# Optimization experiments

Measured on AMD Instinct MI355X. Metric: run time of the kernel, lower is better.

Reference implementation:

```python
import jax, jax.numpy as jnp
import numpy as np

GROUP_SIZE = 128


def dequant_rtn(qweight, scale, zero_point):
    # qweight: [O, I] int, scale/zero_point: [O, I//GROUP_SIZE]
    O, I = qweight.shape
    G = scale.shape[1]
    gs = I // G
    q = qweight.reshape(O, G, gs).astype(jnp.float32)
    zp = zero_point.astype(jnp.float32)[:, :, None]
    w = (q - zp) * scale[:, :, None]
    return w.reshape(O, I)


def setup_inputs() -> dict:
    key = jax.random.key(0)
    k1, k2, k3, k4, k5 = jax.random.split(key, 5)
    B, S, I, O = 2, 2048, 4096, 11008
    G = I // GROUP_SIZE
    x = jax.random.normal(k1, (B, S, I), dtype=jnp.float32)
    qweight = jax.random.randint(k2, (O, I), 0, 16, dtype=jnp.int32)
    scale = jax.random.uniform(k3, (O, G), dtype=jnp.float32) * 0.02 + 1e-3
    zero_point = jax.random.randint(k4, (O, G), 0, 16, dtype=jnp.int32)
    bias = jax.random.normal(k5, (O,), dtype=jnp.float32)
    return {"x": x, "qweight": qweight, "scale": scale,
            "zero_point": zero_point, "bias": bias}


def reference(x, qweight, scale, zero_point, bias):
    # weight-only path: dequant weight, then F.linear(x, w, bias)
    w = dequant_rtn(qweight, scale, zero_point)  # [O, I] fp32
    return jnp.einsum('bsi,oi->bso', x, w) + bias
```

## Files before the change

kernel.cpp:

```cpp
#include <hip/hip_runtime.h>
#include <cstdint>
#include <cstddef>

typedef __attribute__((ext_vector_type(4))) int i32x4;
typedef __bf16 bf16;
typedef __attribute__((ext_vector_type(8))) __bf16 bf16x8;
typedef __attribute__((ext_vector_type(4))) float f32x4;

#define BM 128
#define BN 128
#define BKB 128
#define GROUP_M 16
#define GM256 4
#define NXCD 8

__device__ __forceinline__ unsigned bf16_rne(float f) {
  unsigned u = __float_as_uint(f);
  unsigned r = 0x7FFFu + ((u >> 16) & 1u);
  return ((u + r) >> 16) & 0xFFFFu;
}
__device__ __forceinline__ unsigned pack2(float a, float b) {
  return bf16_rne(a) | (bf16_rne(b) << 16);
}
__device__ __forceinline__ int pack4i8(int a, int b, int c, int d) {
  return (a & 0xFF) | ((b & 0xFF) << 8) | ((c & 0xFF) << 16) | (d << 24);
}
__device__ __forceinline__ int q_i8(float v) {
  v = fminf(fmaxf(v, -127.0f), 127.0f);
  return __float2int_rn(v);
}

__global__ __launch_bounds__(256) void prep_kernel(
    const float* __restrict__ x, char* __restrict__ xq, float* __restrict__ xscale,
    int M,
    const int* __restrict__ q, const float* __restrict__ scale,
    const int* __restrict__ zp, char* __restrict__ wq, float* __restrict__ wscale,
    int K, int G) {
  __shared__ float red[4];
  const int b = blockIdx.x;
  const int tid = threadIdx.x;
  float f[16];

  if (b < M) {
    const float4* src = (const float4*)(x + (size_t)b * K);
#pragma unroll
    for (int i = 0; i < 4; ++i) {
      float4 v = src[tid + 256 * i];
      f[4 * i + 0] = v.x; f[4 * i + 1] = v.y;
      f[4 * i + 2] = v.z; f[4 * i + 3] = v.w;
    }
  } else {
    const int row = b - M;
    const int4* src = (const int4*)(q + (size_t)row * K);
    const float* srow = scale + (size_t)row * G;
    const int*   zrow = zp + (size_t)row * G;
#pragma unroll
    for (int i = 0; i < 4; ++i) {
      const int j = tid + 256 * i;
      const int g = j >> 5;
      const float s = srow[g];
      const float nzs = -s * (float)zrow[g];
      int4 qv = src[j];
      f[4 * i + 0] = fmaf((float)qv.x, s, nzs);
      f[4 * i + 1] = fmaf((float)qv.y, s, nzs);
      f[4 * i + 2] = fmaf((float)qv.z, s, nzs);
      f[4 * i + 3] = fmaf((float)qv.w, s, nzs);
    }
  }

  float m = 0.f;
#pragma unroll
  for (int j = 0; j < 16; ++j) m = fmaxf(m, fabsf(f[j]));
#pragma unroll
  for (int off = 32; off >= 1; off >>= 1) m = fmaxf(m, __shfl_xor(m, off));
  if ((tid & 63) == 0) red[tid >> 6] = m;
  __syncthreads();
  m = fmaxf(fmaxf(red[0], red[1]), fmaxf(red[2], red[3]));

  const float inv = m > 0.f ? 127.0f / m : 0.f;
  int pk[4];
#pragma unroll
  for (int i = 0; i < 4; ++i)
    pk[i] = pack4i8(q_i8(f[4 * i + 0] * inv), q_i8(f[4 * i + 1] * inv),
                    q_i8(f[4 * i + 2] * inv), q_i8(f[4 * i + 3] * inv));

  char* dst = (b < M) ? (xq + (size_t)b * K) : (wq + (size_t)(b - M) * K);
  int* dst_i32 = (int*)dst;
#pragma unroll
  for (int i = 0; i < 4; ++i) dst_i32[tid + 256 * i] = pk[i];

  if (tid == 0) {
    if (b < M) xscale[b] = m * (1.0f / 127.0f);
    else       wscale[b - M] = m * (1.0f / 127.0f);
  }
}

typedef __attribute__((address_space(1))) void gas_void;
typedef __attribute__((address_space(3))) void las_void;

__device__ __forceinline__ void load_lds16(const void* g, void* l) {
  __builtin_amdgcn_global_load_lds((gas_void*)g, (las_void*)l, 16, 0, 0);
}


#define STAGE_A(buf, half, ktb) do {                                          \
    load_lds16(A + abase + (size_t)(half) * 128 * K + (size_t)(ktb) + off0,   \
               &Al[buf][(half) * 16384 + d0w]);                               \
    load_lds16(A + abase + (size_t)(half) * 128 * K + (size_t)(ktb) + off1,   \
               &Al[buf][(half) * 16384 + d1w]);                               \
  } while (0)

#define STAGE_B(buf, half, ktb) do {                                          \
    load_lds16(Bw + bbase + (size_t)(half) * 128 * K + (size_t)(ktb) + off0,  \
               &Bl[buf][(half) * 16384 + d0w]);                               \
    load_lds16(Bw + bbase + (size_t)(half) * 128 * K + (size_t)(ktb) + off1,  \
               &Bl[buf][(half) * 16384 + d1w]);                               \
  } while (0)

#define PHASE(CUR, MH, NH, STAGE_STMT, WAIT_STMT) do {                        \
    i32x4 afr[4][2], bfr[2][2];                                               \
    _Pragma("unroll")                                                         \
    for (int tm = 0; tm < 4; ++tm) {                                          \
      _Pragma("unroll")                                                       \
      for (int ks = 0; ks < 2; ++ks) {                                        \
        int row = wmb + (MH) * 64 + tm * 16 + l16;                            \
        int kq  = ks * 4 + quad;                                              \
        afr[tm][ks] =                                                         \
            *(const i32x4*)&Al[CUR][(row * 8 + (kq ^ (row & 7))) * 16];       \
      }                                                                       \
    }                                                                         \
    _Pragma("unroll")                                                         \
    for (int tn = 0; tn < 2; ++tn) {                                          \
      _Pragma("unroll")                                                       \
      for (int ks = 0; ks < 2; ++ks) {                                        \
        int row = wnb + (NH) * 32 + tn * 16 + l16;                            \
        int kq  = ks * 4 + quad;                                              \
        bfr[tn][ks] =                                                         \
            *(const i32x4*)&Bl[CUR][(row * 8 + (kq ^ (row & 7))) * 16];       \
      }                                                                       \
    }                                                                         \
    STAGE_STMT;                                                               \
    __builtin_amdgcn_s_barrier();                                             \
    asm volatile("s_waitcnt lgkmcnt(0)" ::: "memory");                        \
    __builtin_amdgcn_sched_barrier(0);                                        \
    __builtin_amdgcn_s_setprio(1);                                            \
    _Pragma("unroll")                                                         \
    for (int tm = 0; tm < 4; ++tm) {                                          \
      _Pragma("unroll")                                                       \
      for (int tn = 0; tn < 2; ++tn) {                                        \
        _Pragma("unroll")                                                     \
        for (int ks = 0; ks < 2; ++ks) {                                      \
          acc[(MH) * 4 + tm][(NH) * 2 + tn] =                                 \
              __builtin_amdgcn_mfma_i32_16x16x64_i8(                          \
                  afr[tm][ks], bfr[tn][ks],                                   \
                  acc[(MH) * 4 + tm][(NH) * 2 + tn], 0, 0, 0);                \
        }                                                                     \
      }                                                                       \
    }                                                                         \
    __builtin_amdgcn_s_setprio(0);                                            \
    WAIT_STMT;                                                                \
    __builtin_amdgcn_s_barrier();                                             \
    __builtin_amdgcn_sched_barrier(0);                                        \
  } while (0)

__global__ __launch_bounds__(512) void gemm_i8_256(
    const char* __restrict__ A,
    const char* __restrict__ Bw,
    const float* __restrict__ ascale,
    const float* __restrict__ bscale,
    const float* __restrict__ bias,
    float* __restrict__ C,
    int M, int N, int K) {
  __shared__ __align__(16) char Al[2][256 * 128];
  __shared__ __align__(16) char Bl[2][256 * 128];
  const int tid  = threadIdx.x;
  const int wave = tid >> 6;
  const int lane = tid & 63;
  const int quad = lane >> 4;
  const int l16  = lane & 15;
  const int wmb  = (wave >> 2) * 128;
  const int wnb  = (wave & 3) * 64;

  const int nbm = M / 256, nbn = N / 256;
  const int cpx = (nbm * nbn) / NXCD;
  const int swz = ((int)blockIdx.x % NXCD) * cpx + (int)blockIdx.x / NXCD;
  const int per_group = GM256 * nbn;
  const int gid = swz / per_group;
  const int rem = swz - gid * per_group;
  int gm = nbm - gid * GM256; if (gm > GM256) gm = GM256;
  const int bm = (gid * GM256 + (rem % gm)) * 256;
  const int bn = (rem / gm) * 256;

  const int sA = tid, sB = 512 + tid;
  const int m0 = sA >> 3, m1 = sB >> 3;
  const size_t off0 = (size_t)m0 * K + (size_t)(((sA & 7) ^ (m0 & 7)) * 16);
  const size_t off1 = (size_t)m1 * K + (size_t)(((sB & 7) ^ (m1 & 7)) * 16);
  const int d0w = (0 * 512 + wave * 64) * 16;
  const int d1w = (1 * 512 + wave * 64) * 16;
  const size_t abase = (size_t)bm * K;
  const size_t bbase = (size_t)bn * K;
  const int NT = K / 128;

  i32x4 acc[8][4];
#pragma unroll
  for (int i = 0; i < 8; ++i)
#pragma unroll
    for (int j = 0; j < 4; ++j)
      acc[i][j] = (i32x4){0, 0, 0, 0};

  STAGE_A(0, 0, 0);
  STAGE_A(0, 1, 0);
  STAGE_B(0, 0, 0);
  STAGE_B(0, 1, 0);
  asm volatile("s_waitcnt vmcnt(0)" ::: "memory");
  __builtin_amdgcn_s_barrier();
  __builtin_amdgcn_sched_barrier(0);

  for (int t = 0; t < NT; ++t) {
    const int cur = t & 1;
    const int nxt = cur ^ 1;
    const int kt1 = (t + 1) * 128;
    const bool s1 = (t + 1) < NT;

    PHASE(cur, 0, 0, { if (s1) { STAGE_A(nxt, 0, kt1); STAGE_A(nxt, 1, kt1); } }, {});
    PHASE(cur, 1, 0, { if (s1) { STAGE_B(nxt, 0, kt1); STAGE_B(nxt, 1, kt1); } }, {});
    PHASE(cur, 0, 1, {}, {});
    PHASE(cur, 1, 1, {},
          { asm volatile("s_waitcnt vmcnt(0)" ::: "memory"); });
  }

#pragma unroll
  for (int tn = 0; tn < 4; ++tn) {
    int col = bn + wnb + tn * 16 + l16;
    float bv = bias[col];
    float ws = bscale[col];
#pragma unroll
    for (int tm = 0; tm < 8; ++tm) {
      int row0 = bm + wmb + tm * 16 + quad * 4;
#pragma unroll
      for (int v = 0; v < 4; ++v) {
        float val = ascale[row0 + v] * ws * (float)acc[tm][tn][v] + bv;
        __builtin_nontemporal_store(val, &C[(size_t)(row0 + v) * N + col]);
      }
    }
  }
}

__global__ __launch_bounds__(256) void gemm_i8_kernel(
    const char* __restrict__ A, const char* __restrict__ Bw,
    const float* __restrict__ ascale, const float* __restrict__ bscale,
    const float* __restrict__ bias, float* __restrict__ C,
    int M, int N, int K) {
  __shared__ __align__(16) char Alds[BM * BKB];
  __shared__ __align__(16) char Blds[BN * BKB];
  const int tid  = threadIdx.x;
  const int wave = tid >> 6;
  const int lane = tid & 63;
  const int quad = lane >> 4;
  const int l16  = lane & 15;

  const int nbm = M / BM;
  const int nbn = N / BN;
  int flat = blockIdx.x;
  int per_group = GROUP_M * nbn;
  int gid = flat / per_group;
  int rem = flat - gid * per_group;
  int gm = nbm - gid * GROUP_M;
  if (gm > GROUP_M) gm = GROUP_M;
  const int bm = (gid * GROUP_M + (rem % gm)) * BM;
  const int bn = (rem / gm) * BN;

  const int wm = (wave & 1) * 64;
  const int wn = (wave >> 1) * 64;

  i32x4 acc[4][4];
#pragma unroll
  for (int i = 0; i < 4; ++i)
#pragma unroll
    for (int j = 0; j < 4; ++j)
      acc[i][j] = (i32x4){0, 0, 0, 0};

  for (int kt = 0; kt < K; kt += BKB) {
#pragma unroll
    for (int t = 0; t < 4; ++t) {
      int s0 = (wave * 4 + t) * 64;
      int s  = s0 + lane;
      int m  = s >> 3;
      int kq = (s & 7) ^ (m & 7);
      load_lds16(A  + (size_t)(bm + m) * K + kt + kq * 16, &Alds[s0 * 16]);
      load_lds16(Bw + (size_t)(bn + m) * K + kt + kq * 16, &Blds[s0 * 16]);
    }
    __syncthreads();

#pragma unroll
    for (int ks = 0; ks < 2; ++ks) {
      i32x4 af[4], bfr[4];
#pragma unroll
      for (int tm = 0; tm < 4; ++tm) {
        int m  = wm + tm * 16 + l16;
        int kq = ks * 4 + quad;
        af[tm] = *(const i32x4*)&Alds[(m * 8 + (kq ^ (m & 7))) * 16];
      }
#pragma unroll
      for (int tn = 0; tn < 4; ++tn) {
        int n  = wn + tn * 16 + l16;
        int kq = ks * 4 + quad;
        bfr[tn] = *(const i32x4*)&Blds[(n * 8 + (kq ^ (n & 7))) * 16];
      }
#pragma unroll
      for (int tm = 0; tm < 4; ++tm)
#pragma unroll
        for (int tn = 0; tn < 4; ++tn)
          acc[tm][tn] = __builtin_amdgcn_mfma_i32_16x16x64_i8(
              af[tm], bfr[tn], acc[tm][tn], 0, 0, 0);
    }
    __syncthreads();
  }

#pragma unroll
  for (int tn = 0; tn < 4; ++tn) {
    int col = bn + wn + tn * 16 + l16;
    float bv = bias[col];
    float ws = bscale[col];
#pragma unroll
    for (int tm = 0; tm < 4; ++tm) {
      int row0 = bm + wm + tm * 16 + quad * 4;
#pragma unroll
      for (int v = 0; v < 4; ++v) {
        float val = ascale[row0 + v] * ws * (float)acc[tm][tn][v] + bv;
        __builtin_nontemporal_store(val, &C[(size_t)(row0 + v) * N + col]);
      }
    }
  }
}

__global__ __launch_bounds__(256) void gemm_fused_kernel(
    const float* __restrict__ X, const int* __restrict__ Q,
    const float* __restrict__ scale, const int* __restrict__ zp,
    const float* __restrict__ bias, float* __restrict__ C,
    int M, int N, int K, int G) {
  __shared__ __align__(16) bf16 Alds[128 * 64];
  __shared__ __align__(16) bf16 Blds[128 * 64];
  const int tid  = threadIdx.x;
  const int wave = tid >> 6;
  const int lane = tid & 63;
  const int quad = lane >> 4;
  const int l16  = lane & 15;
  const int bm = blockIdx.y * 128;
  const int bn = blockIdx.x * 128;
  const int wm = (wave & 1) * 64;
  const int wn = (wave >> 1) * 64;

  f32x4 acc[4][4];
#pragma unroll
  for (int i = 0; i < 4; ++i)
#pragma unroll
    for (int j = 0; j < 4; ++j)
      acc[i][j] = (f32x4){0.f, 0.f, 0.f, 0.f};

  for (int kt = 0; kt < K; kt += 64) {
#pragma unroll
    for (int i = 0; i < 4; ++i) {
      int c = tid + i * 256;
      int m = c >> 3;
      int kq = (c & 7) ^ (m & 7);
      const float* src = X + (size_t)(bm + m) * K + kt + kq * 8;
      float4 v0 = *(const float4*)src;
      float4 v1 = *(const float4*)(src + 4);
      uint4 p;
      p.x = pack2(v0.x, v0.y); p.y = pack2(v0.z, v0.w);
      p.z = pack2(v1.x, v1.y); p.w = pack2(v1.z, v1.w);
      *(uint4*)&Alds[c * 8] = p;
    }
#pragma unroll
    for (int i = 0; i < 4; ++i) {
      int c = tid + i * 256;
      int n = c >> 3;
      int kq = (c & 7) ^ (n & 7);
      int kcol = kt + kq * 8;
      size_t row = (size_t)(bn + n);
      int g = kcol >> 7;
      float s = scale[row * G + g];
      float z = (float)zp[row * G + g];
      const int* src = Q + row * K + kcol;
      int4 q0 = *(const int4*)src;
      int4 q1 = *(const int4*)(src + 4);
      uint4 p;
      p.x = pack2(((float)q0.x - z) * s, ((float)q0.y - z) * s);
      p.y = pack2(((float)q0.z - z) * s, ((float)q0.w - z) * s);
      p.z = pack2(((float)q1.x - z) * s, ((float)q1.y - z) * s);
      p.w = pack2(((float)q1.z - z) * s, ((float)q1.w - z) * s);
      *(uint4*)&Blds[c * 8] = p;
    }
    __syncthreads();

#pragma unroll
    for (int ks = 0; ks < 2; ++ks) {
      bf16x8 af[4], bfr[4];
#pragma unroll
      for (int tm = 0; tm < 4; ++tm) {
        int m  = wm + tm * 16 + l16;
        int kq = ks * 4 + quad;
        af[tm] = *(const bf16x8*)&Alds[(m * 8 + (kq ^ (m & 7))) * 8];
      }
#pragma unroll
      for (int tn = 0; tn < 4; ++tn) {
        int n  = wn + tn * 16 + l16;
        int kq = ks * 4 + quad;
        bfr[tn] = *(const bf16x8*)&Blds[(n * 8 + (kq ^ (n & 7))) * 8];
      }
#pragma unroll
      for (int tm = 0; tm < 4; ++tm)
#pragma unroll
        for (int tn = 0; tn < 4; ++tn)
          acc[tm][tn] = __builtin_amdgcn_mfma_f32_16x16x32_bf16(
              af[tm], bfr[tn], acc[tm][tn], 0, 0, 0);
    }
    __syncthreads();
  }

#pragma unroll
  for (int tn = 0; tn < 4; ++tn) {
    int col = bn + wn + tn * 16 + l16;
    float bv = bias[col];
#pragma unroll
    for (int tm = 0; tm < 4; ++tm) {
      int row0 = bm + wm + tm * 16 + quad * 4;
#pragma unroll
      for (int v = 0; v < 4; ++v)
        C[(size_t)(row0 + v) * N + col] = acc[tm][tn][v] + bv;
    }
  }
}

extern "C" void kernel_launch(void* const* d_in, const int* in_sizes, int n_in,
                              void* d_out, int out_size, void* d_ws, size_t ws_size,
                              hipStream_t stream) {
  const float* x     = (const float*)d_in[0];
  const int*   qw    = (const int*)d_in[1];
  const float* scale = (const float*)d_in[2];
  const int*   zp    = (const int*)d_in[3];
  const float* bias  = (const float*)d_in[4];
  float* out = (float*)d_out;

  const int O = in_sizes[4];
  const int I = (int)(in_sizes[1] / O);
  const int M = (int)(in_sizes[0] / I);
  const int G = in_sizes[2] / O;
  const int K = I, N = O;

  size_t off_xq = 0;
  size_t off_xs = off_xq + (size_t)M * K;
  size_t off_wq = (off_xs + (size_t)M * 4 + 255) & ~(size_t)255;
  size_t off_ws_ = off_wq + (size_t)N * K;
  size_t need   = ((off_ws_ + (size_t)N * 4 + 255) & ~(size_t)255);

  if (ws_size >= need && K == 4096) {
    char*  xq = (char*)d_ws + off_xq;
    float* xs = (float*)((char*)d_ws + off_xs);
    char*  wq = (char*)d_ws + off_wq;
    float* wsc = (float*)((char*)d_ws + off_ws_);

    prep_kernel<<<M + N, 256, 0, stream>>>(x, xq, xs, M, qw, scale, zp, wq, wsc, K, G);

    const int nb256 = (M / 256) * (N / 256);
    if ((M % 256) == 0 && (N % 256) == 0 && (nb256 % NXCD) == 0) {
      gemm_i8_256<<<nb256, 512, 0, stream>>>(xq, wq, xs, wsc, bias, out, M, N, K);
    } else {
      int nblocks = (M / BM) * (N / BN);
      gemm_i8_kernel<<<nblocks, 256, 0, stream>>>(xq, wq, xs, wsc, bias, out, M, N, K);
    }
  } else {
    dim3 gemm_grid((unsigned)(N / 128), (unsigned)(M / 128));
    gemm_fused_kernel<<<gemm_grid, 256, 0, stream>>>(x, qw, scale, zp, bias, out,
                                                     M, N, K, G);
  }
}
```

Baseline: 557.5 us.

## Split LDS tiles into quarter-stages and prefetch two K-steps ahead

Reorganizes the A and B LDS layouts into halves indexed by which phase consumes them. Each half is refilled as soon as the phase reading it finishes, so the loads for step t+2 are issued into the current buffer while step t is still computing. The waits become partial (vmcnt(4)) instead of full drains, which deepens the pipeline and hides more global load latency. The cost is more involved buffer-reuse ordering, which relies on correct barrier placement to avoid overwriting data before every wave has read it.

Result: no change. 563.2 us (+1.0%).

```diff
diff --git a/kernel.cpp b/kernel.cpp
--- a/kernel.cpp
+++ b/kernel.cpp
@@ -103,18 +103,18 @@
 }
 
 
-#define STAGE_A(buf, half, ktb) do {                                          \
-    load_lds16(A + abase + (size_t)(half) * 128 * K + (size_t)(ktb) + off0,   \
-               &Al[buf][(half) * 16384 + d0w]);                               \
-    load_lds16(A + abase + (size_t)(half) * 128 * K + (size_t)(ktb) + off1,   \
-               &Al[buf][(half) * 16384 + d1w]);                               \
+#define STAGE_A_H(buf, h, ktb) do {                                           \
+    load_lds16(A + abase + (size_t)(ktb) + aoff0 + (size_t)(h) * 64 * K,      \
+               &Al[buf][(h) * 8192 + dw]);                                    \
+    load_lds16(A + abase + (size_t)(ktb) + aoff1 + (size_t)(h) * 64 * K,      \
+               &Al[buf][16384 + (h) * 8192 + dw]);                            \
   } while (0)
 
-#define STAGE_B(buf, half, ktb) do {                                          \
-    load_lds16(Bw + bbase + (size_t)(half) * 128 * K + (size_t)(ktb) + off0,  \
-               &Bl[buf][(half) * 16384 + d0w]);                               \
-    load_lds16(Bw + bbase + (size_t)(half) * 128 * K + (size_t)(ktb) + off1,  \
-               &Bl[buf][(half) * 16384 + d1w]);                               \
+#define STAGE_B_H(buf, h, ktb) do {                                           \
+    load_lds16(Bw + bbase + (size_t)(ktb) + boff0 + (size_t)(h) * 32 * K,     \
+               &Bl[buf][(h) * 16384 + dw]);                                   \
+    load_lds16(Bw + bbase + (size_t)(ktb) + boff1 + (size_t)(h) * 32 * K,     \
+               &Bl[buf][(h) * 16384 + 8192 + dw]);                            \
   } while (0)
 
 #define PHASE(CUR, MH, NH, STAGE_STMT, WAIT_STMT) do {                        \
@@ -133,10 +133,10 @@
     for (int tn = 0; tn < 2; ++tn) {                                          \
       _Pragma("unroll")                                                       \
       for (int ks = 0; ks < 2; ++ks) {                                        \
-        int row = wnb + (NH) * 32 + tn * 16 + l16;                            \
-        int kq  = ks * 4 + quad;                                              \
+        int p  = (NH) * 128 + wq3 * 32 + tn * 16 + l16;                       \
+        int kq = ks * 4 + quad;                                               \
         bfr[tn][ks] =                                                         \
-            *(const i32x4*)&Bl[CUR][(row * 8 + (kq ^ (row & 7))) * 16];       \
+            *(const i32x4*)&Bl[CUR][(p * 8 + (kq ^ (p & 7))) * 16];           \
       }                                                                       \
     }                                                                         \
     STAGE_STMT;                                                               \
@@ -178,8 +178,9 @@
   const int lane = tid & 63;
   const int quad = lane >> 4;
   const int l16  = lane & 15;
+  const int wq3  = wave & 3;
   const int wmb  = (wave >> 2) * 128;
-  const int wnb  = (wave & 3) * 64;
+  const int wnb  = wq3 * 64;
 
   const int nbm = M / 256, nbn = N / 256;
   const int cpx = (nbm * nbn) / NXCD;
@@ -191,12 +192,13 @@
   const int bm = (gid * GM256 + (rem % gm)) * 256;
   const int bn = (rem / gm) * 256;
 
-  const int sA = tid, sB = 512 + tid;
-  const int m0 = sA >> 3, m1 = sB >> 3;
-  const size_t off0 = (size_t)m0 * K + (size_t)(((sA & 7) ^ (m0 & 7)) * 16);
-  const size_t off1 = (size_t)m1 * K + (size_t)(((sB & 7) ^ (m1 & 7)) * 16);
-  const int d0w = (0 * 512 + wave * 64) * 16;
-  const int d1w = (1 * 512 + wave * 64) * 16;
+  const int r0 = tid >> 3;
+  const int kq16 = (((tid & 7) ^ (r0 & 7)) * 16);
+  const size_t aoff0 = (size_t)r0 * K + kq16;
+  const size_t aoff1 = aoff0 + (size_t)128 * K;
+  const size_t boff0 = (size_t)((r0 >> 5) * 64 + (r0 & 31)) * K + kq16;
+  const size_t boff1 = boff0 + (size_t)128 * K;
+  const int dw = wave * 1024;
   const size_t abase = (size_t)bm * K;
   const size_t bbase = (size_t)bn * K;
   const int NT = K / 128;
@@ -208,11 +210,13 @@
     for (int j = 0; j < 4; ++j)
       acc[i][j] = (i32x4){0, 0, 0, 0};
 
-  STAGE_A(0, 0, 0);
-  STAGE_A(0, 1, 0);
-  STAGE_B(0, 0, 0);
-  STAGE_B(0, 1, 0);
-  asm volatile("s_waitcnt vmcnt(0)" ::: "memory");
+  STAGE_A_H(0, 0, 0);
+  STAGE_A_H(0, 1, 0);
+  STAGE_B_H(0, 0, 0);
+  STAGE_B_H(0, 1, 0);
+  STAGE_B_H(1, 0, 128);
+  STAGE_A_H(1, 0, 128);
+  asm volatile("s_waitcnt vmcnt(4)" ::: "memory");
   __builtin_amdgcn_s_barrier();
   __builtin_amdgcn_sched_barrier(0);
 
@@ -220,13 +224,18 @@
     const int cur = t & 1;
     const int nxt = cur ^ 1;
     const int kt1 = (t + 1) * 128;
+    const int kt2 = (t + 2) * 128;
     const bool s1 = (t + 1) < NT;
-
-    PHASE(cur, 0, 0, { if (s1) { STAGE_A(nxt, 0, kt1); STAGE_A(nxt, 1, kt1); } }, {});
-    PHASE(cur, 1, 0, { if (s1) { STAGE_B(nxt, 0, kt1); STAGE_B(nxt, 1, kt1); } }, {});
-    PHASE(cur, 0, 1, {}, {});
-    PHASE(cur, 1, 1, {},
-          { asm volatile("s_waitcnt vmcnt(0)" ::: "memory"); });
+    const bool s2 = (t + 2) < NT;
+
+    PHASE(cur, 0, 0, { if (s1) STAGE_A_H(nxt, 1, kt1); }, {});
+    PHASE(cur, 1, 0, { if (s1) STAGE_B_H(nxt, 1, kt1); }, {});
+    PHASE(cur, 0, 1, { if (s2) STAGE_B_H(cur, 0, kt2); }, {});
+    PHASE(cur, 1, 1, { if (s2) STAGE_A_H(cur, 0, kt2); },
+          {
+            if (s2) { asm volatile("s_waitcnt vmcnt(4)" ::: "memory"); }
+            else    { asm volatile("s_waitcnt vmcnt(0)" ::: "memory"); }
+          });
   }
 
 #pragma unroll
```
